# Performance work log

Hardware: AMD Instinct MI355X
Metric: run time of the kernel (lower is better)

## Reference

```python
import jax, jax.numpy as jnp
import numpy as np

N_FREQ = 5
K = 16  # nneigh


def _gather(points, idx):
    # points: [B,N,C], idx: [B,nQ,K] -> [B,nQ,K,C]
    return jax.vmap(lambda p, i: p[i])(points, idx)


def setup_inputs() -> dict:
    key = jax.random.key(0)
    ks = jax.random.split(key, 16)
    B, nQ, N, dim_inp, dim = 2, 8192, 4096, 128, 128
    s = dim_inp ** -0.5
    return {
        "xyz_q": jax.random.uniform(ks[0], (B, nQ, 2), jnp.float32),
        "lat_rep": jax.random.normal(ks[1], (B, dim_inp), jnp.float32),
        "xyz": jax.random.uniform(ks[2], (B, N, 3), jnp.float32),
        "points": jax.random.normal(ks[3], (B, N, dim_inp), jnp.float32),
        "w_qs": jax.random.normal(ks[4], (dim_inp, dim), jnp.float32) * s,
        "w_ks": jax.random.normal(ks[5], (dim_inp, dim), jnp.float32) * s,
        "w_vs": jax.random.normal(ks[6], (dim_inp, dim), jnp.float32) * s,
        "w_kg": jax.random.normal(ks[7], (dim_inp, dim), jnp.float32) * s,
        "w_vg": jax.random.normal(ks[8], (dim_inp, dim), jnp.float32) * s,
        "gamma_w1": jax.random.normal(ks[9], (dim, dim), jnp.float32) * (dim ** -0.5),
        "gamma_b1": jnp.zeros((dim,), jnp.float32),
        "gamma_w2": jax.random.normal(ks[10], (dim, dim), jnp.float32) * (dim ** -0.5),
        "gamma_b2": jnp.zeros((dim,), jnp.float32),
        "pe_w": jax.random.normal(ks[11], (3 * 2 * N_FREQ + 3, dim), jnp.float32) * (33 ** -0.5),
        "pe_b": jnp.zeros((dim,), jnp.float32),
    }


def reference(xyz_q, lat_rep, xyz, points, w_qs, w_ks, w_vs, w_kg, w_vg,
              gamma_w1, gamma_b1, gamma_w2, gamma_b2, pe_w, pe_b):
    b, nQ, _ = xyz_q.shape
    dim = w_qs.shape[1]
    # kNN in 2D (no_grad in original): squared distance [B,nQ,N]
    dists = jnp.sum((xyz_q[:, :, None] - xyz[:, None, :, :2]) ** 2, axis=-1)
    _, knn_idx = jax.lax.top_k(-dists, K)  # ascending distance order

    # global latent [B,dim_inp] branch
    q_attn = (lat_rep @ w_qs)[:, None, None, :]          # [B,1,1,dim]
    k_global = jnp.broadcast_to((lat_rep @ w_kg)[:, None, None, :], (b, nQ, 1, dim))
    v_global = jnp.broadcast_to((lat_rep @ w_vg)[:, None, None, :], (b, nQ, 1, dim))

    k_attn = jnp.concatenate([_gather(points @ w_ks, knn_idx), k_global], axis=2)  # [B,nQ,K+1,dim]
    v_attn = jnp.concatenate([_gather(points @ w_vs, knn_idx), v_global], axis=2)

    xyz_knn = _gather(xyz, knn_idx)                      # [B,nQ,K,3]
    pos_diff = jnp.concatenate(
        [xyz_q[:, :, None] - xyz_knn[..., :2], xyz_knn[..., -1:]], axis=-1)  # [B,nQ,K,3]
    freq_bands = jnp.linspace(1.0, 2.0 ** N_FREQ, N_FREQ)
    embeds = [pos_diff]
    for fr in freq_bands:
        embeds.append(jnp.sin(pos_diff * fr))
        embeds.append(jnp.cos(pos_diff * fr))
    pos_embed = jnp.concatenate(embeds, axis=-1)         # [B,nQ,K,33]
    pos_encode = pos_embed @ pe_w + pe_b                 # [B,nQ,K,dim]
    pos_encode = jnp.concatenate(
        [pos_encode, jnp.zeros((b, nQ, 1, dim), pos_encode.dtype)], axis=2)  # [B,nQ,K+1,dim]

    h = q_attn - k_attn + pos_encode
    h = jnp.maximum(h @ gamma_w1 + gamma_b1, 0.0) @ gamma_w2 + gamma_b2
    attn = jax.nn.softmax(h, axis=-2)                    # softmax over neighbor axis
    res = jnp.sum(attn * (v_attn + pos_encode), axis=2)  # einsum 'bmnf,bmnf->bmf'
    return res
```

## Files before the change

### kernel.cpp

```cpp
#include <hip/hip_runtime.h>
#include <cstdint>

#define DIM   128
#define KNN   16
#define NB    2
#define NQ    8192
#define NPTS  4096
#define KVROWS 16
#define GRID  32
#define NCELL (GRID*GRID)
#define CAP   384

typedef unsigned short ushort_t;
typedef short vshort8 __attribute__((ext_vector_type(8)));
typedef float vfloat4 __attribute__((ext_vector_type(4)));

__device__ __forceinline__ ushort_t bf16_rne(float f) {
    unsigned u = __float_as_uint(f);
    unsigned r = u + 0x7FFFu + ((u >> 16) & 1u);
    return (ushort_t)(r >> 16);
}
__device__ __forceinline__ int cell_of(float x) {
    int c = (int)(x * 32.0f);
    return min(max(c, 0), GRID - 1);
}

__device__ __forceinline__ void pack_body(
    const float* __restrict__ src, int K, int ncols, int NT, int KS,
    ushort_t* __restrict__ dst, int gid)
{
    int total = NT*KS*64;
    if (gid >= total) return;
    int lane = gid & 63; int c = gid >> 6;
    int s = c % KS; int n = c / KS;
    int k0 = s*32 + ((lane >> 4) << 3);
    int col = n*16 + (lane & 15);
    vshort8 v;
    #pragma unroll
    for (int i = 0; i < 8; ++i) {
        int k = k0 + i;
        float f = (k < K) ? src[k*ncols + col] : 0.f;
        v[i] = (short)bf16_rne(f);
    }
    *(vshort8*)(dst + gid*8) = v;
}

__device__ __forceinline__ void scan1024(
    const int* __restrict__ cnt, int* __restrict__ cs, int* __restrict__ cu,
    int* __restrict__ ss, int t)
{
    int v0 = cnt[t*4 + 0];
    int v1 = cnt[t*4 + 1];
    int v2 = cnt[t*4 + 2];
    int v3 = cnt[t*4 + 3];
    int p0 = v0, p1 = p0 + v1, p2 = p1 + v2, p3 = p2 + v3;
    ss[t] = p3;
    __syncthreads();
    for (int off = 1; off < 256; off <<= 1) {
        int add = (t >= off) ? ss[t - off] : 0;
        __syncthreads();
        ss[t] += add;
        __syncthreads();
    }
    int excl = ss[t] - p3;
    cs[t*4 + 0] = excl;        cu[t*4 + 0] = excl;
    cs[t*4 + 1] = excl + p0;   cu[t*4 + 1] = excl + p0;
    cs[t*4 + 2] = excl + p1;   cu[t*4 + 2] = excl + p1;
    cs[t*4 + 3] = excl + p2;   cu[t*4 + 3] = excl + p2;
    if (t == 255) cs[NCELL] = ss[255];
}

__global__ __launch_bounds__(256) void pre1_k(
    const float* __restrict__ w_ks, const float* __restrict__ g_w1,
    const float* __restrict__ pe_w, const float* __restrict__ xyz,
    const float* __restrict__ xyz_q,
    float* __restrict__ Wk1, float* __restrict__ pwc,
    int* __restrict__ cellcnt, int* __restrict__ qcnt)
{
    int t = threadIdx.x; int bx = blockIdx.x;
    if (bx < 64) {
        int row = bx*2 + (t >> 7); int f = t & 127;
        float acc = 0.f;
        for (int c = 0; c < 128; ++c) acc = fmaf(w_ks[row*128 + c], g_w1[c*128 + f], acc);
        Wk1[row*128 + f] = acc;
    } else if (bx < 128) {
        int r = bx - 64; int col = t;
        float v = 0.f;
        if (r < 33) {
            if (col < 128) {
                float a = 0.f;
                for (int c = 0; c < 128; ++c) a = fmaf(pe_w[r*128 + c], g_w1[c*128 + col], a);
                v = a;
            } else {
                v = pe_w[r*128 + (col - 128)];
            }
        }
        pwc[r*256 + col] = v;
    } else if (bx < 160) {
        int gid = (bx - 128)*256 + t;
        int b = gid >> 12; int n = gid & (NPTS - 1);
        const float* p = xyz + (b*NPTS + n)*3;
        atomicAdd(&cellcnt[b*NCELL + cell_of(p[1])*GRID + cell_of(p[0])], 1);
    } else {
        int gid = (bx - 160)*256 + t;
        int b = gid >> 13; int q = gid & (NQ - 1);
        const float* p = xyz_q + (b*NQ + q)*2;
        atomicAdd(&qcnt[b*NCELL + cell_of(p[1])*GRID + cell_of(p[0])], 1);
    }
}

__global__ __launch_bounds__(256) void pre2_k(
    const float* __restrict__ pwc, const float* __restrict__ g_w2,
    const int* __restrict__ cnt, const int* __restrict__ qcnt,
    const float* __restrict__ lat, const float* __restrict__ w_qs,
    const float* __restrict__ w_kg, const float* __restrict__ w_vg,
    const float* __restrict__ g_w1, const float* __restrict__ g_b1,
    const float* __restrict__ pe_b,
    ushort_t* __restrict__ pwf, ushort_t* __restrict__ w2f,
    int* __restrict__ cell_start, int* __restrict__ cursor,
    int* __restrict__ qstart, int* __restrict__ qcursor,
    float* __restrict__ c1_out, float* __restrict__ vg_out, float* __restrict__ h2g_out)
{
    __shared__ int ss[256];
    __shared__ float qs[NB][DIM];
    __shared__ float hgx[NB][DIM];
    __shared__ float h1gx[NB][DIM];
    int t = threadIdx.x; int bx = blockIdx.x;
    if (bx < 4) {
        pack_body(pwc, 32, 256, 16, 1, pwf, bx*256 + t);
    } else if (bx < 12) {
        pack_body(g_w2, 128, 128, 8, 4, w2f, (bx - 4)*256 + t);
    } else if (bx < 14) {
        int b = bx - 12;
        scan1024(cnt + b*NCELL, cell_start + b*(NCELL+1), cursor + b*NCELL, ss, t);
    } else if (bx < 16) {
        int b = bx - 14;
        scan1024(qcnt + b*NCELL, qstart + b*(NCELL+1), qcursor + b*NCELL, ss, t);
    } else {
        int b = t >> 7; int f = t & 127;
        float aq = 0.f, ak = 0.f, av = 0.f;
        for (int c = 0; c < DIM; ++c) {
            float l = lat[b*DIM + c];
            aq = fmaf(l, w_qs[c*DIM + f], aq);
            ak = fmaf(l, w_kg[c*DIM + f], ak);
            av = fmaf(l, w_vg[c*DIM + f], av);
        }
        vg_out[b*DIM + f] = av;
        qs[b][f] = aq + pe_b[f];
        hgx[b][f] = aq - ak;
        __syncthreads();
        float acc = g_b1[f], acch = g_b1[f];
        for (int c = 0; c < DIM; ++c) {
            float w = g_w1[c*DIM + f];
            acc  = fmaf(qs[b][c], w, acc);
            acch = fmaf(hgx[b][c], w, acch);
        }
        c1_out[b*DIM + f] = acc;
        h1gx[b][f] = fmaxf(acch, 0.f);
        __syncthreads();
        float acc2 = 0.f;
        for (int c = 0; c < DIM; ++c) acc2 = fmaf(h1gx[b][c], g_w2[c*DIM + f], acc2);
        h2g_out[b*DIM + f] = acc2;
    }
}

__global__ __launch_bounds__(256) void pre3_k(
    const float* __restrict__ points, const float* __restrict__ Wk1,
    const float* __restrict__ w_vs, const float* __restrict__ pe_b,
    const float* __restrict__ xyz, const float* __restrict__ xyz_q,
    int* __restrict__ cursor, int* __restrict__ qcursor,
    float* __restrict__ K1p, float* __restrict__ Vp,
    float2* __restrict__ sxy, int* __restrict__ sidx,
    float2* __restrict__ qsxy, int* __restrict__ qsidx)
{
    __shared__ __align__(16) float pts[KVROWS*DIM];
    int t = threadIdx.x; int bx = blockIdx.x;
    if (bx < 512) {
        int r0 = bx * KVROWS;
        #pragma unroll
        for (int k = 0; k < KVROWS*DIM/256; ++k) {
            int e = t + k*256;
            pts[e] = points[r0*DIM + e];
        }
        __syncthreads();
        int f = t & 127; int mat = t >> 7;
        const float* W = mat ? w_vs : Wk1;
        float* O = mat ? Vp : K1p;
        float addv = mat ? pe_b[f] : 0.f;
        float acc[KVROWS];
        #pragma unroll
        for (int r = 0; r < KVROWS; ++r) acc[r] = 0.f;
        const float4* pts4 = reinterpret_cast<const float4*>(pts);
        for (int c4 = 0; c4 < DIM/4; ++c4) {
            float w0 = W[(c4*4+0)*DIM + f];
            float w1 = W[(c4*4+1)*DIM + f];
            float w2 = W[(c4*4+2)*DIM + f];
            float w3 = W[(c4*4+3)*DIM + f];
            #pragma unroll
            for (int r = 0; r < KVROWS; ++r) {
                float4 p = pts4[r*(DIM/4) + c4];
                acc[r] = fmaf(p.x, w0, acc[r]);
                acc[r] = fmaf(p.y, w1, acc[r]);
                acc[r] = fmaf(p.z, w2, acc[r]);
                acc[r] = fmaf(p.w, w3, acc[r]);
            }
        }
        #pragma unroll
        for (int r = 0; r < KVROWS; ++r) O[(r0 + r)*DIM + f] = acc[r] + addv;
    } else if (bx < 544) {
        int gid = (bx - 512)*256 + t;
        int b = gid >> 12; int n = gid & (NPTS - 1);
        const float* p = xyz + (b*NPTS + n)*3;
        float x = p[0], y = p[1];
        int slot = atomicAdd(&cursor[b*NCELL + cell_of(y)*GRID + cell_of(x)], 1);
        sxy[b*NPTS + slot] = make_float2(x, y);
        sidx[b*NPTS + slot] = n;
    } else {
        int gid = (bx - 544)*256 + t;
        int b = gid >> 13; int q = gid & (NQ - 1);
        const float* p = xyz_q + (b*NQ + q)*2;
        float x = p[0], y = p[1];
        int slot = atomicAdd(&qcursor[b*NCELL + cell_of(y)*GRID + cell_of(x)], 1);
        qsxy[b*NQ + slot] = make_float2(x, y);
        qsidx[b*NQ + slot] = q;
    }
}

__global__ __launch_bounds__(256) void knn_k(
    const float2* __restrict__ qsxy, const float2* __restrict__ sxy,
    const int* __restrict__ sidx, const int* __restrict__ cstart,
    int* __restrict__ knn_out)
{
    __shared__ float cand_d[4][CAP];
    __shared__ int   cand_i[4][CAP];
    int t = threadIdx.x; int wid = t >> 6, lane = t & 63;
    int bx = blockIdx.x; int b = bx >> 11; int q = (bx & 2047)*4 + wid;
    float2 qp = qsxy[b*NQ + q];
    float xq = qp.x, yq = qp.y;
    int cx = cell_of(xq), cy = cell_of(yq);
    const int* cs_b = cstart + b*(NCELL+1);
    float* cd = cand_d[wid]; int* ci = cand_i[wid];
    const float INF = 3.4e38f;
    const float CS = 1.0f/32.0f;
    int* outp = knn_out + (b*NQ + q)*KNN;
    int myIdx = 0;

    for (int R = 2; R < 9; ++R) {
        int x0 = max(cx-R, 0), x1 = min(cx+R, GRID-1);
        int y0 = max(cy-R, 0), y1 = min(cy+R, GRID-1);
        int cnt = 0;
        for (int ry = y0; ry <= y1; ++ry) {
            int s0 = cs_b[ry*GRID + x0];
            int e0 = cs_b[ry*GRID + x1 + 1];
            for (int o = s0 + lane; o < e0; o += 64) {
                float2 p = sxy[b*NPTS + o];
                float dx = __fadd_rn(xq, -p.x);
                float dy = __fadd_rn(yq, -p.y);
                float d = __fadd_rn(__fmul_rn(dx, dx), __fmul_rn(dy, dy));
                int slot = cnt + (o - s0);
                if (slot < CAP) { cd[slot] = d; ci[slot] = o; }
            }
            cnt += e0 - s0;
        }
        asm volatile("s_waitcnt lgkmcnt(0)" ::: "memory");
        __builtin_amdgcn_sched_barrier(0);

        float dr[6];
        #pragma unroll
        for (int k = 0; k < 6; ++k)
            dr[k] = (lane + k*64 < cnt) ? cd[lane + k*64] : INF;
        float d16 = INF;
        for (int r = 0; r < KNN; ++r) {
            float v = dr[0]; int s = lane;
            #pragma unroll
            for (int k = 1; k < 6; ++k)
                if (dr[k] < v) { v = dr[k]; s = lane + k*64; }
            #pragma unroll
            for (int off = 32; off >= 1; off >>= 1) {
                float ov = __shfl_xor(v, off);
                int   os = __shfl_xor(s, off);
                if (ov < v || (ov == v && os < s)) { v = ov; s = os; }
            }
            if (lane == r) myIdx = sidx[b*NPTS + ci[s]];
            if ((s & 63) == lane) {
                int k = s >> 6;
                if      (k == 0) dr[0] = INF;
                else if (k == 1) dr[1] = INF;
                else if (k == 2) dr[2] = INF;
                else if (k == 3) dr[3] = INF;
                else if (k == 4) dr[4] = INF;
                else             dr[5] = INF;
            }
            d16 = v;
        }
        float bl = (x0 > 0)      ? (xq - (float)x0*CS)       : INF;
        float br = (x1 < GRID-1) ? ((float)(x1+1)*CS - xq)   : INF;
        float bb = (y0 > 0)      ? (yq - (float)y0*CS)       : INF;
        float bt = (y1 < GRID-1) ? ((float)(y1+1)*CS - yq)   : INF;
        float safe = fminf(fminf(bl, br), fminf(bb, bt)) - 2e-6f;
        bool whole = (safe > 1e8f);
        bool ok = (cnt >= KNN) && (cnt <= CAP) && (whole || d16 <= safe*safe);
        if (ok || R == 8) {
            if (lane < KNN) outp[lane] = myIdx;
            break;
        }
    }
}

__global__ __launch_bounds__(512, 2) void fuse_k(
    const float2* __restrict__ qsxy, const int* __restrict__ qsidx,
    const float* __restrict__ xyz,
    const float* __restrict__ K1p, const float* __restrict__ Vp,
    const int* __restrict__ knn_idx,
    const float* __restrict__ c1_, const float* __restrict__ vg_,
    const float* __restrict__ h2g_, const float* __restrict__ pw32_,
    const ushort_t* __restrict__ pwf, const ushort_t* __restrict__ w2f,
    float* __restrict__ out)
{
    __shared__ __align__(16) ushort_t w2B[32*512];
    __shared__ __align__(16) ushort_t h1b[8][2048];

    int t = threadIdx.x, lane = t & 63, wid = t >> 6;
    int sid = (blockIdx.x & 7) * 64 + (blockIdx.x >> 3);
    int b = sid >> 8; int qbase = (sid & 255) * 32;

    {
        const int4* s2 = (const int4*)w2f;  int4* d2 = (int4*)w2B;
        #pragma unroll
        for (int i = 0; i < 4; ++i) d2[t + i*512] = s2[t + i*512];
    }
    __syncthreads();

    int c16 = lane & 15, g = lane >> 4, rowbase = g*4;
    ushort_t* hb = h1b[wid];
    const vshort8* pwBv = (const vshort8*)pwf;
    const vshort8* w2Bv = (const vshort8*)w2B;
    const vfloat4 vzero = (vfloat4){0.f, 0.f, 0.f, 0.f};

    float pw32r[16], c1r[8], hgr[8], vgr[8];
    #pragma unroll
    for (int n = 0; n < 16; ++n) pw32r[n] = pw32_[n*16 + c16];
    #pragma unroll
    for (int n = 0; n < 8; ++n) {
        c1r[n] = c1_[b*128 + n*16 + c16];
        hgr[n] = h2g_[b*128 + n*16 + c16];
        vgr[n] = vg_[b*128 + n*16 + c16];
    }

    #pragma unroll 1
    for (int qi = 0; qi < 4; ++qi) {
        int q = qbase + wid*4 + qi;
        float2 qp = qsxy[b*NQ + q];
        float xq = qp.x, yq = qp.y;
        int qorig = qsidx[b*NQ + q];
        int idxrow = knn_idx[(b*NQ + q)*KNN + c16];
        const float* p = xyz + (b*NPTS + idxrow)*3;
        float pd0 = xq - p[0], pd1 = yq - p[1], pd2 = p[2];
        int idxr[4];
        #pragma unroll
        for (int r = 0; r < 4; ++r) idxr[r] = __shfl(idxrow, rowbase + r);

        vshort8 eh;
        int k0 = g*8;
        #pragma unroll
        for (int j = 0; j < 8; ++j) {
            int k = k0 + j;
            float v;
            if (k < 3) {
                v = (k == 0) ? pd0 : (k == 1 ? pd1 : pd2);
            } else {
                int m = k - 3; int fi = m / 6; int rem = m - fi*6;
                int comp = (rem < 3) ? rem : rem - 3;
                float pdc = (comp == 0) ? pd0 : (comp == 1 ? pd1 : pd2);
                float fr = (fi == 0) ? 1.0f : (fi == 1) ? 8.75f : (fi == 2) ? 16.5f
                         : (fi == 3) ? 24.25f : 32.0f;
                float arg = pdc * fr;
                v = (rem < 3) ? __sinf(arg) : __cosf(arg);
            }
            eh[j] = (short)bf16_rne(v);
        }
        float c32 = __cosf(32.0f * pd2);
        float c32r[4];
        #pragma unroll
        for (int r = 0; r < 4; ++r) c32r[r] = __shfl(c32, rowbase + r);

        float k1v[4][8];
        #pragma unroll
        for (int r = 0; r < 4; ++r) {
            const float* kp = K1p + ((b*NPTS + idxr[r]) << 7) + c16;
            #pragma unroll
            for (int n = 0; n < 8; ++n) k1v[r][n] = kp[n*16];
        }

        #pragma unroll
        for (int n = 0; n < 8; ++n) {
            vfloat4 a = __builtin_amdgcn_mfma_f32_16x16x32_bf16(
                eh, pwBv[n*64 + lane], vzero, 0, 0, 0);
            int col = n*16 + c16;
            int s = col >> 5;
            int lp = ((col >> 3) & 3) << 4;
            int j = c16 & 7;
            #pragma unroll
            for (int r = 0; r < 4; ++r) {
                float h = c1r[n] - k1v[r][n] + fmaf(c32r[r], pw32r[n], a[r]);
                h = fmaxf(h, 0.f);
                hb[s*512 + (lp | (rowbase + r))*8 + j] = bf16_rne(h);
            }
        }
        asm volatile("s_waitcnt lgkmcnt(0)" ::: "memory");
        __builtin_amdgcn_sched_barrier(0);

        vfloat4 acc2[8];
        #pragma unroll
        for (int n = 0; n < 8; ++n) acc2[n] = vzero;
        #pragma unroll
        for (int s = 0; s < 4; ++s) {
            vshort8 ah = ((const vshort8*)hb)[s*64 + lane];
            #pragma unroll
            for (int n = 0; n < 8; ++n) {
                vshort8 bh = w2Bv[(n*4 + s)*64 + lane];
                acc2[n] = __builtin_amdgcn_mfma_f32_16x16x32_bf16(ah, bh, acc2[n], 0, 0, 0);
            }
        }

        const float* vbase[4];
        #pragma unroll
        for (int r = 0; r < 4; ++r) vbase[r] = Vp + ((b*NPTS + idxr[r]) << 7) + c16;
        float vvp[4];
        #pragma unroll
        for (int r = 0; r < 4; ++r) vvp[r] = vbase[r][0];

        #pragma unroll
        for (int n = 0; n < 8; ++n) {
            float vvc[4];
            #pragma unroll
            for (int r = 0; r < 4; ++r) vvc[r] = vvp[r];
            if (n < 7) {
                #pragma unroll
                for (int r = 0; r < 4; ++r) vvp[r] = vbase[r][(n+1)*16];
            }
            vfloat4 ap = __builtin_amdgcn_mfma_f32_16x16x32_bf16(
                eh, pwBv[(8 + n)*64 + lane], vzero, 0, 0, 0);
            #pragma unroll
            for (int r = 0; r < 4; ++r) ap[r] = fmaf(c32r[r], pw32r[8 + n], ap[r]);

            float hg = hgr[n];
            vfloat4 a2 = acc2[n];
            float mx = fmaxf(fmaxf(a2[0], a2[1]), fmaxf(a2[2], a2[3]));
            mx = fmaxf(mx, __shfl_xor(mx, 16));
            mx = fmaxf(mx, __shfl_xor(mx, 32));
            mx = fmaxf(mx, hg);
            float sum = 0.f, num = 0.f;
            #pragma unroll
            for (int r = 0; r < 4; ++r) {
                float ev = __expf(a2[r] - mx);
                float v = vvc[r] + ap[r];
                sum += ev;
                num = fmaf(ev, v, num);
            }
            sum += __shfl_xor(sum, 16); sum += __shfl_xor(sum, 32);
            num += __shfl_xor(num, 16); num += __shfl_xor(num, 32);
            float eg = __expf(hg - mx);
            sum += eg;
            num = fmaf(eg, vgr[n], num);
            if (g == 0) out[(b*NQ + qorig)*128 + n*16 + c16] = num / sum;
        }
        asm volatile("s_waitcnt lgkmcnt(0)" ::: "memory");
        __builtin_amdgcn_sched_barrier(0);
    }
}

extern "C" void kernel_launch(void* const* d_in, const int* in_sizes, int n_in,
                              void* d_out, int out_size, void* d_ws, size_t ws_size,
                              hipStream_t stream) {
    const float* xyz_q  = (const float*)d_in[0];
    const float* lat    = (const float*)d_in[1];
    const float* xyz    = (const float*)d_in[2];
    const float* points = (const float*)d_in[3];
    const float* w_qs   = (const float*)d_in[4];
    const float* w_ks   = (const float*)d_in[5];
    const float* w_vs   = (const float*)d_in[6];
    const float* w_kg   = (const float*)d_in[7];
    const float* w_vg   = (const float*)d_in[8];
    const float* g_w1   = (const float*)d_in[9];
    const float* g_b1   = (const float*)d_in[10];
    const float* g_w2   = (const float*)d_in[11];
    const float* g_b2   = (const float*)d_in[12];
    const float* pe_w   = (const float*)d_in[13];
    const float* pe_b   = (const float*)d_in[14];
    float* out = (float*)d_out;
    (void)g_b2;

    float* ws   = (float*)d_ws;
    float* Vp   = ws;
    float* K1p  = Vp  + NB*NPTS*DIM;
    float* Wk1  = K1p + NB*NPTS*DIM;
    float* pwc  = Wk1 + DIM*DIM;
    float* c1   = pwc + 64*256;
    float* vg   = c1  + NB*DIM;
    float* h2g  = vg  + NB*DIM;
    int*   knn  = (int*)(h2g + NB*DIM);
    ushort_t* pwf = (ushort_t*)(knn + NB*NQ*KNN);
    ushort_t* w2f = pwf + 16*64*8;
    int* cellcnt  = (int*)(w2f + 32*64*8);
    int* qcnt     = cellcnt + NB*NCELL;
    int* cellstart = qcnt + NB*NCELL;
    int* cursor    = cellstart + NB*(NCELL+1);
    int* qstart    = cursor + NB*NCELL;
    int* qcursor   = qstart + NB*(NCELL+1);
    int* sidx      = qcursor + NB*NCELL;
    float2* sxy    = (float2*)(sidx + NB*NPTS);
    int* qsidx     = (int*)(sxy + NB*NPTS);
    float2* qsxy   = (float2*)(qsidx + NB*NQ);

    hipMemsetAsync(cellcnt, 0, 2*NB*NCELL*sizeof(int), stream);
    pre1_k<<<224, 256, 0, stream>>>(w_ks, g_w1, pe_w, xyz, xyz_q,
                                    Wk1, pwc, cellcnt, qcnt);
    pre2_k<<<17, 256, 0, stream>>>(pwc, g_w2, cellcnt, qcnt,
                                   lat, w_qs, w_kg, w_vg, g_w1, g_b1, pe_b,
                                   pwf, w2f, cellstart, cursor, qstart, qcursor,
                                   c1, vg, h2g);
    pre3_k<<<608, 256, 0, stream>>>(points, Wk1, w_vs, pe_b, xyz, xyz_q,
                                    cursor, qcursor, K1p, Vp, sxy, sidx, qsxy, qsidx);
    knn_k<<<NB*NQ/4, 256, 0, stream>>>(qsxy, sxy, sidx, cellstart, knn);
    fuse_k<<<NB*NQ/32, 512, 0, stream>>>(qsxy, qsidx, xyz, K1p, Vp, knn, c1, vg, h2g,
                                         pwc + 32*256, pwf, w2f, out);
}
```

Baseline: 136.2 us.

## Replace iterative argmin kNN selection with ballot-based threshold binary search

In the kNN kernel, the 16 rounds of wave-wide argmin (each a shuffle reduction) are replaced. The new code binary-searches the float bit pattern of a distance threshold, counting the candidates under it with ballot and popcount. Points below the threshold, then points equal to it, are compacted into the output with ballot prefix sums. This cuts the shuffle work and serial rounds, but the neighbors are no longer written in ascending distance order. That is harmless only because the downstream softmax-weighted sum is order-invariant.

```diff
diff --git a/kernel.cpp b/kernel.cpp
--- a/kernel.cpp
+++ b/kernel.cpp
@@ -243,7 +243,7 @@
     const float INF = 3.4e38f;
     const float CS = 1.0f/32.0f;
     int* outp = knn_out + (b*NQ + q)*KNN;
-    int myIdx = 0;
+    unsigned long long lmask = (1ull << lane) - 1ull;
 
     for (int R = 2; R < 9; ++R) {
         int x0 = max(cx-R, 0), x1 = min(cx+R, GRID-1);
@@ -265,43 +265,56 @@
         asm volatile("s_waitcnt lgkmcnt(0)" ::: "memory");
         __builtin_amdgcn_sched_barrier(0);
 
+        int cc = min(cnt, CAP);
         float dr[6];
         #pragma unroll
         for (int k = 0; k < 6; ++k)
-            dr[k] = (lane + k*64 < cnt) ? cd[lane + k*64] : INF;
-        float d16 = INF;
-        for (int r = 0; r < KNN; ++r) {
-            float v = dr[0]; int s = lane;
-            #pragma unroll
-            for (int k = 1; k < 6; ++k)
-                if (dr[k] < v) { v = dr[k]; s = lane + k*64; }
-            #pragma unroll
-            for (int off = 32; off >= 1; off >>= 1) {
-                float ov = __shfl_xor(v, off);
-                int   os = __shfl_xor(s, off);
-                if (ov < v || (ov == v && os < s)) { v = ov; s = os; }
-            }
-            if (lane == r) myIdx = sidx[b*NPTS + ci[s]];
-            if ((s & 63) == lane) {
-                int k = s >> 6;
-                if      (k == 0) dr[0] = INF;
-                else if (k == 1) dr[1] = INF;
-                else if (k == 2) dr[2] = INF;
-                else if (k == 3) dr[3] = INF;
-                else if (k == 4) dr[4] = INF;
-                else             dr[5] = INF;
-            }
-            d16 = v;
-        }
+            dr[k] = (lane + k*64 < cc) ? cd[lane + k*64] : INF;
+
+        unsigned lo = 0u, hi = 0x40000000u;
+        #pragma unroll 1
+        for (int it = 0; it < 32; ++it) {
+            if (hi - lo <= 1u) break;
+            unsigned mid = (lo + hi) >> 1;
+            float pv = __uint_as_float(mid);
+            int c = 0;
+            #pragma unroll
+            for (int k = 0; k < 6; ++k)
+                c += __popcll(__ballot(dr[k] <= pv));
+            if (c >= KNN) {
+                hi = mid;
+                if (c == KNN) break;
+            } else {
+                lo = mid;
+            }
+        }
+        float thr = __uint_as_float(hi);
+
         float bl = (x0 > 0)      ? (xq - (float)x0*CS)       : INF;
         float br = (x1 < GRID-1) ? ((float)(x1+1)*CS - xq)   : INF;
         float bb = (y0 > 0)      ? (yq - (float)y0*CS)       : INF;
         float bt = (y1 < GRID-1) ? ((float)(y1+1)*CS - yq)   : INF;
         float safe = fminf(fminf(bl, br), fminf(bb, bt)) - 2e-6f;
         bool whole = (safe > 1e8f);
-        bool ok = (cnt >= KNN) && (cnt <= CAP) && (whole || d16 <= safe*safe);
+        bool ok = (cnt >= KNN) && (cnt <= CAP) && (whole || thr <= safe*safe);
         if (ok || R == 8) {
-            if (lane < KNN) outp[lane] = myIdx;
+            int base = 0;
+            #pragma unroll
+            for (int k = 0; k < 6; ++k) {
+                bool p = dr[k] < thr;
+                unsigned long long m = __ballot(p);
+                int pos = base + __popcll(m & lmask);
+                if (p && pos < KNN) outp[pos] = sidx[b*NPTS + ci[lane + k*64]];
+                base += __popcll(m);
+            }
+            #pragma unroll
+            for (int k = 0; k < 6; ++k) {
+                bool p = dr[k] == thr;
+                unsigned long long m = __ballot(p);
+                int pos = base + __popcll(m & lmask);
+                if (p && pos < KNN) outp[pos] = sidx[b*NPTS + ci[lane + k*64]];
+                base += __popcll(m);
+            }
             break;
         }
     }
```

Result: faster. 109.7 us (-19.4%).
